# Optimization experiments

Measured on AMD Instinct MI355X. Metric: run time of the kernel, lower is better.

The kernel has to match this reference:

```python
import jax, jax.numpy as jnp
import numpy as np

NUM_HEADS = 16
GROUP_SIZE = 4
RMS_EPS = 1e-6


def _rope_cos_sin(S, head_dim):
    # matches compute_freqs_cis: freqs = 1/10000**(arange(0,hd,2)/hd), angles = outer(t, freqs)
    inv_freq = 1.0 / (10000.0 ** (jnp.arange(0, head_dim, 2, dtype=jnp.float32) / head_dim))
    t = jnp.arange(S, dtype=jnp.float32)
    angles = t[:, None] * inv_freq[None, :]          # [S, hd/2]
    return jnp.cos(angles), jnp.sin(angles)


def _apply_rope(x, cos, sin):
    # x: [B, S, h, hd]; complex multiply on (even, odd) pairs
    B, S, h, hd = x.shape
    xr = x.reshape(B, S, h, hd // 2, 2)
    x0, x1 = xr[..., 0], xr[..., 1]
    c = cos[None, :, None, :]
    s = sin[None, :, None, :]
    o0 = x0 * c - x1 * s
    o1 = x0 * s + x1 * c
    return jnp.stack([o0, o1], axis=-1).reshape(B, S, h, hd)


def setup_inputs() -> dict:
    key = jax.random.key(0)
    k1, k2, k3 = jax.random.split(key, 3)
    B, S, H = 4, 2048, 2048
    g = GROUP_SIZE
    x = jax.random.normal(k1, (B, S, H), dtype=jnp.float32)
    w_attn = jax.random.normal(k2, (H, H + 2 * H // g), dtype=jnp.float32) * 0.02
    w_proj = jax.random.normal(k3, (H, H), dtype=jnp.float32) * 0.02
    norm_w = jnp.ones((H,), dtype=jnp.float32)
    return {"x": x, "w_attn": w_attn, "w_proj": w_proj, "norm_w": norm_w}


def reference(x, w_attn, w_proj, norm_w):
    B, S, H = x.shape
    nh = NUM_HEADS
    g = GROUP_SIZE
    nkv = nh // g
    hd = H // nh
    ghd = H // g

    qkv = jnp.einsum('bsh,hf->bsf', x, w_attn)
    q = qkv[..., :H].reshape(B, S, nh, hd)
    k = qkv[..., H:H + ghd].reshape(B, S, nkv, hd)
    v = qkv[..., H + ghd:].reshape(B, S, nkv, hd)

    cos, sin = _rope_cos_sin(S, hd)
    q = _apply_rope(q, cos, sin)
    k = _apply_rope(k, cos, sin)

    q = q.transpose(0, 2, 1, 3)                      # [B, nh, S, hd]
    k = jnp.repeat(k.transpose(0, 2, 1, 3), g, axis=1)   # [B, nh, S, hd]
    v = jnp.repeat(v.transpose(0, 2, 1, 3), g, axis=1)

    scale = 1.0 / jnp.sqrt(jnp.float32(hd))
    scores = jnp.einsum('bhqd,bhkd->bhqk', q, k) * scale
    causal = jnp.tril(jnp.ones((S, S), dtype=bool))
    scores = jnp.where(causal[None, None], scores, jnp.finfo(scores.dtype).min)
    attn = jax.nn.softmax(scores, axis=-1)
    y = jnp.einsum('bhqk,bhkd->bhqd', attn, v)       # [B, nh, S, hd]
    y = y.transpose(0, 2, 1, 3).reshape(B, S, H)

    y = jnp.einsum('bsh,ho->bso', y, w_proj)
    # RMSNorm
    rms = jnp.sqrt(jnp.mean(jnp.square(y), axis=-1, keepdims=True) + RMS_EPS)
    return (y / rms) * norm_w
```

## Files before the change

kernel.cpp:

```cpp
#include <hip/hip_runtime.h>

#define DEVI __device__ __forceinline__

using u16 = unsigned short;
using u32 = unsigned int;

typedef __attribute__((ext_vector_type(8))) short short8v;
typedef __attribute__((ext_vector_type(4))) float f32x4;
typedef __attribute__((ext_vector_type(16))) float f32x16;
typedef __attribute__((ext_vector_type(2))) u32 u32x2;
typedef __attribute__((ext_vector_type(4))) u32 u32x4;

DEVI u16 f2b(float f) {
  u32 u = __builtin_bit_cast(u32, f);
  u += 0x7fffu + ((u >> 16) & 1u);
  return (u16)(u >> 16);
}
DEVI float b2f(u16 b) { return __builtin_bit_cast(float, (u32)b << 16); }

DEVI void gload16(const void* g, void* l) {
  __builtin_amdgcn_global_load_lds(
      (const __attribute__((address_space(1))) void*)g,
      (__attribute__((address_space(3))) void*)l, 16, 0, 0);
}

__global__ __launch_bounds__(256) void cvt_x_k(const float* __restrict__ in,
                                               u16* __restrict__ out) {
  size_t i = ((size_t)blockIdx.x * 256 + threadIdx.x) * 8;
  f32x4 a = *(const f32x4*)(in + i);
  f32x4 c = *(const f32x4*)(in + i + 4);
  short8v o;
  o[0] = (short)f2b(a[0]); o[1] = (short)f2b(a[1]);
  o[2] = (short)f2b(a[2]); o[3] = (short)f2b(a[3]);
  o[4] = (short)f2b(c[0]); o[5] = (short)f2b(c[1]);
  o[6] = (short)f2b(c[2]); o[7] = (short)f2b(c[3]);
  *(short8v*)(out + i) = o;
}

__global__ __launch_bounds__(256) void transpose_cvt_k(
    const float* __restrict__ in, u16* __restrict__ out, int R, int Ccols) {
  __shared__ u16 tile[64][65];
  const int r0 = blockIdx.y * 64, c0 = blockIdx.x * 64;
  const int tx = threadIdx.x & 63, ty = threadIdx.x >> 6;
#pragma unroll
  for (int jj = 0; jj < 16; ++jj) {
    int r = ty + jj * 4;
    tile[r][tx] = f2b(in[(size_t)(r0 + r) * Ccols + c0 + tx]);
  }
  __syncthreads();
#pragma unroll
  for (int jj = 0; jj < 16; ++jj) {
    int c = ty + jj * 4;
    out[(size_t)(c0 + c) * R + r0 + tx] = tile[tx][c];
  }
}

__global__ __launch_bounds__(256) void rope_table_k(float* __restrict__ cosT,
                                                    float* __restrict__ sinT) {
  int idx = blockIdx.x * 256 + threadIdx.x;
  int s = idx >> 6, i = idx & 63;
  float inv_freq = expf(-(float)i * (1.0f / 64.0f) * 9.210340371976184f);
  float ang = (float)s * inv_freq;
  cosT[idx] = cosf(ang);
  sinT[idx] = sinf(ang);
}

__global__ __launch_bounds__(256) void rope_scatter_k(
    const u16* __restrict__ qkv, const float* __restrict__ cosT,
    const float* __restrict__ sinT, u16* __restrict__ q_r,
    u16* __restrict__ k_r) {
  const float QS = 0.08838834764831845f * 1.4426950408889634f;
  const int row = blockIdx.x;
  const int b = row >> 11, s = row & 2047;
  const u16* in = qkv + (size_t)row * 3072;
  const float* cp = cosT + s * 64;
  const float* sp = sinT + s * 64;
  for (int p = threadIdx.x; p < 1280; p += 256) {
    int f0 = p * 2;
    u32 pair = *(const u32*)(in + f0);
    float x0 = b2f((u16)(pair & 0xffffu));
    float x1 = b2f((u16)(pair >> 16));
    int d, head;
    u16* dst;
    bool isq = (f0 < 2048);
    if (isq) {
      head = f0 >> 7; d = f0 & 127;
      dst = q_r + (((size_t)(b * 16 + head)) * 2048 + s) * 128 + d;
    } else {
      int idx = f0 - 2048;
      head = idx >> 7; d = idx & 127;
      dst = k_r + (((size_t)(b * 4 + head)) * 2048 + s) * 128 + d;
    }
    int i = d >> 1;
    float c = cp[i], sn = sp[i];
    float o0 = x0 * c - x1 * sn;
    float o1 = x0 * sn + x1 * c;
    if (isq) { o0 *= QS; o1 *= QS; }
    *(u32*)dst = (u32)f2b(o0) | ((u32)f2b(o1) << 16);
  }
}

__global__ __launch_bounds__(256) void v_trans_k(const u16* __restrict__ qkv,
                                                 u16* __restrict__ vT) {
  __shared__ u16 tile[64][65];
  const int s0 = blockIdx.x * 64, d0 = blockIdx.y * 64;
  const int bk = blockIdx.z;
  const int b = bk >> 2, kh = bk & 3;
  const int tx = threadIdx.x & 63, ty = threadIdx.x >> 6;
  const u16* src = qkv + ((size_t)b * 2048) * 3072 + 2560 + kh * 128;
#pragma unroll
  for (int jj = 0; jj < 16; ++jj) {
    int s = ty + jj * 4;
    tile[s][tx] = src[(size_t)(s0 + s) * 3072 + d0 + tx];
  }
  __syncthreads();
  u16* dst = vT + (((size_t)bk * 128 + d0) * 2048) + s0;
#pragma unroll
  for (int jj = 0; jj < 16; ++jj) {
    int dd = ty + jj * 4;
    dst[(size_t)dd * 2048 + tx] = tile[tx][dd];
  }
}

DEVI short8v ldf(const char* half, int r, int slot) {
  return *(const short8v*)(half + r * 64 + (((slot) ^ (r & 3)) << 4));
}

DEVI void stg(const u16* __restrict__ G, int row0, int Kd, int T, int kh,
              char* dst, int t, int w) {
#pragma unroll
  for (int i = 0; i < 2; ++i) {
    int off = i * 8192 + t * 16;
    int r = off >> 6;
    int gs = ((off >> 4) & 3) ^ (r & 3);
    gload16((const char*)G +
                (((size_t)(row0 + r) * Kd) + T * 64 + kh * 32 + gs * 8) * 2,
            dst + i * 8192 + w * 1024);
  }
}

#define VM4 asm volatile("s_waitcnt vmcnt(4)" ::: "memory")
#define PH(P2, KS, CH, STAGE_STMT, TAILWAIT)                                   \
  {                                                                            \
    if ((CH) == 0) {                                                           \
      _Pragma("unroll") for (int mt = 0; mt < 8; ++mt) af[mt] =                \
          ldf(Ab + (P2) * 32768 + (KS) * 16384, wm * 128 + mt * 16 + lo, hi);  \
    }                                                                          \
    bf0 = ldf(Bb + (P2) * 32768 + (KS) * 16384, wn * 64 + (CH) * 32 + lo, hi);\
    bf1 = ldf(Bb + (P2) * 32768 + (KS) * 16384,                                \
              wn * 64 + (CH) * 32 + 16 + lo, hi);                              \
    STAGE_STMT;                                                                \
    __builtin_amdgcn_sched_barrier(0);                                         \
    __builtin_amdgcn_s_barrier();                                              \
    asm volatile("s_waitcnt lgkmcnt(0)" ::: "memory");                         \
    __builtin_amdgcn_sched_barrier(0);                                         \
    __builtin_amdgcn_s_setprio(1);                                             \
    _Pragma("unroll") for (int mt = 0; mt < 8; ++mt) {                         \
      acc[mt][(CH) * 2] = __builtin_amdgcn_mfma_f32_16x16x32_bf16(             \
          af[mt], bf0, acc[mt][(CH) * 2], 0, 0, 0);                            \
      acc[mt][(CH) * 2 + 1] = __builtin_amdgcn_mfma_f32_16x16x32_bf16(         \
          af[mt], bf1, acc[mt][(CH) * 2 + 1], 0, 0, 0);                        \
    }                                                                          \
    __builtin_amdgcn_s_setprio(0);                                             \
    TAILWAIT;                                                                  \
    __builtin_amdgcn_sched_barrier(0);                                         \
    __builtin_amdgcn_s_barrier();                                              \
    __builtin_amdgcn_sched_barrier(0);                                         \
  }

__global__ __launch_bounds__(512, 2) void gemm256_k(const u16* __restrict__ A,
                                                    const u16* __restrict__ BT,
                                                    u16* __restrict__ C, int N,
                                                    int Kd) {
  __shared__ __align__(16) char lds[131072];
  char* Ab = lds;
  char* Bb = lds + 65536;

  const int t = threadIdx.x;
  const int lane = t & 63, lo = lane & 15, hi = lane >> 4;
  const int w = t >> 6, wm = w >> 2, wn = w & 3;

  const int ntx = gridDim.x;
  const int nwg = ntx * gridDim.y;
  const int orig = blockIdx.y * ntx + blockIdx.x;
  const int cpx = nwg >> 3;
  const int swz = (orig & 7) * cpx + (orig >> 3);
  const int m0 = (swz / ntx) * 256, n0 = (swz % ntx) * 256;

  f32x4 acc[8][4];
#pragma unroll
  for (int a = 0; a < 8; ++a)
#pragma unroll
    for (int c = 0; c < 4; ++c) acc[a][c] = (f32x4){0.f, 0.f, 0.f, 0.f};

  short8v af[8], bf0, bf1;

  const int NK = Kd >> 6;
  const int NK2 = NK >> 1;

  stg(A, m0, Kd, 0, 0, Ab + 0, t, w);
  stg(BT, n0, Kd, 0, 0, Bb + 0, t, w);
  stg(A, m0, Kd, 0, 1, Ab + 16384, t, w);
  stg(BT, n0, Kd, 0, 1, Bb + 16384, t, w);
  stg(A, m0, Kd, 1, 0, Ab + 32768, t, w);
  stg(BT, n0, Kd, 1, 0, Bb + 32768, t, w);
  VM4;
  __builtin_amdgcn_sched_barrier(0);
  __builtin_amdgcn_s_barrier();
  __builtin_amdgcn_sched_barrier(0);

  for (int kt2 = 0; kt2 < NK2; ++kt2) {
    int T1v = 2 * kt2 + 1;
    int T2v = 2 * kt2 + 2; if (T2v > NK - 1) T2v = NK - 1;
    int T3v = 2 * kt2 + 3; if (T3v > NK - 1) T3v = NK - 1;
    PH(0, 0, 0, stg(A, m0, Kd, T1v, 1, Ab + 49152, t, w), (void)0);
    PH(0, 0, 1, stg(BT, n0, Kd, T1v, 1, Bb + 49152, t, w), (void)0);
    PH(0, 1, 0, stg(A, m0, Kd, T2v, 0, Ab + 0, t, w), (void)0);
    PH(0, 1, 1, stg(BT, n0, Kd, T2v, 0, Bb + 0, t, w), VM4);
    PH(1, 0, 0, stg(A, m0, Kd, T2v, 1, Ab + 16384, t, w), (void)0);
    PH(1, 0, 1, stg(BT, n0, Kd, T2v, 1, Bb + 16384, t, w), (void)0);
    PH(1, 1, 0, stg(A, m0, Kd, T3v, 0, Ab + 32768, t, w), (void)0);
    PH(1, 1, 1, stg(BT, n0, Kd, T3v, 0, Bb + 32768, t, w), VM4);
  }
  asm volatile("s_waitcnt vmcnt(0)" ::: "memory");

#pragma unroll
  for (int mt = 0; mt < 8; ++mt)
#pragma unroll
    for (int nt = 0; nt < 4; ++nt)
#pragma unroll
      for (int r = 0; r < 4; ++r) {
        int row = m0 + wm * 128 + mt * 16 + hi * 4 + r;
        int col = n0 + wn * 64 + nt * 16 + lo;
        C[(size_t)row * N + col] = f2b(acc[mt][nt][r]);
      }
}

__global__ __launch_bounds__(256, 3) void attn_k(const u16* __restrict__ Q,
                                                 const u16* __restrict__ K,
                                                 const u16* __restrict__ VT,
                                                 u16* __restrict__ Y) {
  __shared__ __align__(16) u16 lK[2][64 * 128];
  __shared__ __align__(16) u16 lV[128 * 64];

  const int t = threadIdx.x;
  const int lane = t & 63;
  const int l31 = lane & 31, hb = lane >> 5;
  const int w = t >> 6;

  const int id = blockIdx.x;
  const int xcd = id & 7, pos = id >> 3;
  const int bh = xcd + ((pos >> 4) << 3);
  const int qt = 15 - (pos & 15);
  const int b = bh >> 4, h = bh & 15, kh = h >> 2;

  const size_t qbase = (size_t)(b * 16 + h) * 2048 * 128;
  const size_t kbase = (size_t)(b * 4 + kh) * 2048 * 128;
  const size_t vbase = (size_t)(b * 4 + kh) * 128 * 2048;

  const int q0 = qt * 128;
  const int qrow = q0 + w * 32 + l31;

  short8v qf[8];
#pragma unroll
  for (int j16 = 0; j16 < 8; ++j16)
    qf[j16] = *(const short8v*)(Q + qbase + (size_t)qrow * 128 + j16 * 16 + hb * 8);

  float m_run = -3.0e38f, l_run = 0.f;
  f32x16 oacc[4];
#pragma unroll
  for (int db = 0; db < 4; ++db)
#pragma unroll
    for (int rg = 0; rg < 16; ++rg) oacc[db][rg] = 0.f;

  const int ntile = 2 * qt + 2;

  auto stageK = [&](int buf, int j) {
    const int kv0 = j * 64;
#pragma unroll
    for (int i = 0; i < 4; ++i) {
      int off = i * 4096 + t * 16;
      int r = off >> 8;
      int sl = (off >> 4) & 15;
      int gs = sl ^ (r & 7);
      gload16((const char*)K + (kbase + (size_t)(kv0 + r) * 128 + gs * 8) * 2,
              (char*)lK[buf] + i * 4096 + w * 1024);
    }
  };
  auto stageV = [&](int j) {
    const int kv0 = j * 64;
#pragma unroll
    for (int i = 0; i < 4; ++i) {
      int off = i * 4096 + t * 16;
      int r = off >> 7;
      int sl = (off >> 4) & 7;
      int gs = sl ^ (r & 7);
      gload16((const char*)VT + (vbase + (size_t)r * 2048 + kv0 + gs * 8) * 2,
              (char*)lV + i * 4096 + w * 1024);
    }
  };

  stageK(0, 0);
  stageV(0);
  asm volatile("s_waitcnt vmcnt(0)" ::: "memory");
  __builtin_amdgcn_sched_barrier(0);
  __builtin_amdgcn_s_barrier();
  __builtin_amdgcn_sched_barrier(0);

  for (int jj = 0; jj < ntile; ++jj) {
    const int cur = jj & 1;
    const bool pre = (jj + 1 < ntile);
    if (pre) stageK(cur ^ 1, jj + 1);

    const char* lKc = (const char*)lK[cur];
    const int kv0 = jj * 64;

    f32x16 sacc[2];
#pragma unroll
    for (int kb = 0; kb < 2; ++kb)
#pragma unroll
      for (int rg = 0; rg < 16; ++rg) sacc[kb][rg] = 0.f;

    __builtin_amdgcn_s_setprio(1);
#pragma unroll
    for (int j16 = 0; j16 < 8; ++j16) {
      const int c = j16 * 2 + hb;
#pragma unroll
      for (int kb = 0; kb < 2; ++kb) {
        int kr = kb * 32 + l31;
        short8v kf = *(const short8v*)(lKc + kr * 256 + ((c ^ (kr & 7)) << 4));
        sacc[kb] = __builtin_amdgcn_mfma_f32_32x32x16_bf16(kf, qf[j16],
                                                           sacc[kb], 0, 0, 0);
      }
    }
    __builtin_amdgcn_s_setprio(0);

    if (jj >= ntile - 2) {
      const int mb = kv0 + 4 * hb - qrow;
#pragma unroll
      for (int kb = 0; kb < 2; ++kb)
#pragma unroll
        for (int rg = 0; rg < 16; ++rg)
          if (mb + kb * 32 + (rg & 3) + 8 * (rg >> 2) > 0)
            sacc[kb][rg] = -1.0e38f;
    }

    float mt0[16];
#pragma unroll
    for (int rg = 0; rg < 16; ++rg) mt0[rg] = fmaxf(sacc[0][rg], sacc[1][rg]);
#pragma unroll
    for (int rg = 0; rg < 8; ++rg) mt0[rg] = fmaxf(mt0[rg], mt0[rg + 8]);
#pragma unroll
    for (int rg = 0; rg < 4; ++rg) mt0[rg] = fmaxf(mt0[rg], mt0[rg + 4]);
    float mx = fmaxf(fmaxf(mt0[0], mt0[1]), fmaxf(mt0[2], mt0[3]));
    mx = fmaxf(mx, __shfl_xor(mx, 32, 64));

    if (__any(mx > m_run + 8.f)) {
      float mn = fmaxf(m_run, mx);
      float corr = exp2f(m_run - mn);
      m_run = mn;
      l_run *= corr;
#pragma unroll
      for (int db = 0; db < 4; ++db)
#pragma unroll
        for (int rg = 0; rg < 16; ++rg) oacc[db][rg] *= corr;
    }

    float sm0[16];
#pragma unroll
    for (int kb = 0; kb < 2; ++kb)
#pragma unroll
      for (int rg = 0; rg < 16; ++rg)
        sacc[kb][rg] = exp2f(sacc[kb][rg] - m_run);
#pragma unroll
    for (int rg = 0; rg < 16; ++rg) sm0[rg] = sacc[0][rg] + sacc[1][rg];
#pragma unroll
    for (int rg = 0; rg < 8; ++rg) sm0[rg] += sm0[rg + 8];
#pragma unroll
    for (int rg = 0; rg < 4; ++rg) sm0[rg] += sm0[rg + 4];
    float sm = (sm0[0] + sm0[1]) + (sm0[2] + sm0[3]);
    sm += __shfl_xor(sm, 32, 64);
    l_run += sm;

    short8v pa[4];
#pragma unroll
    for (int kb = 0; kb < 2; ++kb) {
      u32 pw00, pw01, pw10, pw11, pw20, pw21, pw30, pw31;
      asm("v_cvt_pk_bf16_f32 %0, %1, %2" : "=v"(pw00) : "v"(sacc[kb][0]), "v"(sacc[kb][1]));
      asm("v_cvt_pk_bf16_f32 %0, %1, %2" : "=v"(pw01) : "v"(sacc[kb][2]), "v"(sacc[kb][3]));
      asm("v_cvt_pk_bf16_f32 %0, %1, %2" : "=v"(pw10) : "v"(sacc[kb][4]), "v"(sacc[kb][5]));
      asm("v_cvt_pk_bf16_f32 %0, %1, %2" : "=v"(pw11) : "v"(sacc[kb][6]), "v"(sacc[kb][7]));
      asm("v_cvt_pk_bf16_f32 %0, %1, %2" : "=v"(pw20) : "v"(sacc[kb][8]), "v"(sacc[kb][9]));
      asm("v_cvt_pk_bf16_f32 %0, %1, %2" : "=v"(pw21) : "v"(sacc[kb][10]), "v"(sacc[kb][11]));
      asm("v_cvt_pk_bf16_f32 %0, %1, %2" : "=v"(pw30) : "v"(sacc[kb][12]), "v"(sacc[kb][13]));
      asm("v_cvt_pk_bf16_f32 %0, %1, %2" : "=v"(pw31) : "v"(sacc[kb][14]), "v"(sacc[kb][15]));
      u32x2 a0 = __builtin_amdgcn_permlane32_swap(pw00, pw10, false, false);
      u32x2 a1 = __builtin_amdgcn_permlane32_swap(pw01, pw11, false, false);
      u32x4 wv0; wv0[0] = a0[0]; wv0[1] = a1[0]; wv0[2] = a0[1]; wv0[3] = a1[1];
      pa[kb * 2 + 0] = __builtin_bit_cast(short8v, wv0);
      u32x2 b0 = __builtin_amdgcn_permlane32_swap(pw20, pw30, false, false);
      u32x2 b1 = __builtin_amdgcn_permlane32_swap(pw21, pw31, false, false);
      u32x4 wv1; wv1[0] = b0[0]; wv1[1] = b1[0]; wv1[2] = b0[1]; wv1[3] = b1[1];
      pa[kb * 2 + 1] = __builtin_bit_cast(short8v, wv1);
    }

    if (pre) { asm volatile("s_waitcnt vmcnt(4)" ::: "memory"); }
    else     { asm volatile("s_waitcnt vmcnt(0)" ::: "memory"); }
    __builtin_amdgcn_sched_barrier(0);
    __builtin_amdgcn_s_barrier();
    __builtin_amdgcn_sched_barrier(0);

    __builtin_amdgcn_s_setprio(1);
#pragma unroll
    for (int sc = 0; sc < 4; ++sc) {
      const int c = sc * 2 + hb;
#pragma unroll
      for (int db = 0; db < 4; ++db) {
        int vr = db * 32 + l31;
        short8v vf = *(const short8v*)((const char*)lV + vr * 128 +
                                       ((c ^ (vr & 7)) << 4));
        oacc[db] = __builtin_amdgcn_mfma_f32_32x32x16_bf16(vf, pa[sc],
                                                           oacc[db], 0, 0, 0);
      }
    }
    __builtin_amdgcn_s_setprio(0);

    asm volatile("s_waitcnt vmcnt(0)" ::: "memory");
    __builtin_amdgcn_sched_barrier(0);
    __builtin_amdgcn_s_barrier();
    __builtin_amdgcn_sched_barrier(0);

    if (pre) stageV(jj + 1);
  }

  const float inv = 1.0f / l_run;
  u16* yp = Y + ((size_t)b * 2048 + qrow) * 2048 + h * 128;
#pragma unroll
  for (int db = 0; db < 4; ++db)
#pragma unroll
    for (int j = 0; j < 4; ++j) {
      float a0 = oacc[db][4 * j] * inv, a1 = oacc[db][4 * j + 1] * inv;
      float a2 = oacc[db][4 * j + 2] * inv, a3 = oacc[db][4 * j + 3] * inv;
      u32 w0, w1;
      asm("v_cvt_pk_bf16_f32 %0, %1, %2" : "=v"(w0) : "v"(a0), "v"(a1));
      asm("v_cvt_pk_bf16_f32 %0, %1, %2" : "=v"(w1) : "v"(a2), "v"(a3));
      *(u32x2*)(yp + db * 32 + 8 * j + 4 * hb) = (u32x2){w0, w1};
    }
}

__global__ __launch_bounds__(256) void rmsnorm_k(const u16* __restrict__ Yb,
                                                 const float* __restrict__ nw,
                                                 float* __restrict__ out) {
  const int row = blockIdx.x;
  const int t = threadIdx.x;
  const u16* yr = Yb + (size_t)row * 2048 + t * 8;
  short8v v = *(const short8v*)yr;
  float x[8];
  float ss = 0.f;
#pragma unroll
  for (int j = 0; j < 8; ++j) {
    x[j] = b2f((u16)v[j]);
    ss += x[j] * x[j];
  }
#pragma unroll
  for (int dm = 1; dm < 64; dm <<= 1) ss += __shfl_xor(ss, dm, 64);
  __shared__ float red[4];
  if ((t & 63) == 0) red[t >> 6] = ss;
  __syncthreads();
  float tot = red[0] + red[1] + red[2] + red[3];
  float inv = rsqrtf(tot * (1.0f / 2048.0f) + 1e-6f);
  float* op = out + (size_t)row * 2048 + t * 8;
  const float* wp = nw + t * 8;
  f32x4 o0, o1;
#pragma unroll
  for (int j = 0; j < 4; ++j) o0[j] = x[j] * inv * wp[j];
#pragma unroll
  for (int j = 0; j < 4; ++j) o1[j] = x[4 + j] * inv * wp[4 + j];
  *(f32x4*)op = o0;
  *(f32x4*)(op + 4) = o1;
}

extern "C" void kernel_launch(void* const* d_in, const int* in_sizes, int n_in,
                              void* d_out, int out_size, void* d_ws,
                              size_t ws_size, hipStream_t stream) {
  (void)in_sizes; (void)n_in; (void)out_size; (void)ws_size;
  const float* x = (const float*)d_in[0];
  const float* w_attn = (const float*)d_in[1];
  const float* w_proj = (const float*)d_in[2];
  const float* norm_w = (const float*)d_in[3];
  float* out = (float*)d_out;
  char* ws = (char*)d_ws;

  size_t off = 0;
  auto alloc = [&](size_t n) {
    size_t r = off;
    off += (n + 255) & ~(size_t)255;
    return r;
  };
  u16* xb = (u16*)(ws + alloc(33554432));
  u16* wabT = (u16*)(ws + alloc(12582912));
  u16* qkv = (u16*)(ws + alloc(50331648));
  u16* q_r = (u16*)(ws + alloc(33554432));
  u16* vT = (u16*)(ws + alloc(8388608));
  u16* wpT = (u16*)(ws + alloc(8388608));
  float* cosT = (float*)(ws + alloc(524288));
  float* sinT = (float*)(ws + alloc(524288));
  u16* k_r = wabT;
  u16* y = xb;
  u16* y2 = qkv;

  cvt_x_k<<<8192, 256, 0, stream>>>(x, xb);
  transpose_cvt_k<<<dim3(48, 32), 256, 0, stream>>>(w_attn, wabT, 2048, 3072);
  transpose_cvt_k<<<dim3(32, 32), 256, 0, stream>>>(w_proj, wpT, 2048, 2048);
  rope_table_k<<<512, 256, 0, stream>>>(cosT, sinT);
  gemm256_k<<<dim3(12, 32), 512, 0, stream>>>(xb, wabT, qkv, 8192 == 0 ? 0 : 3072, 2048);
  rope_scatter_k<<<8192, 256, 0, stream>>>(qkv, cosT, sinT, q_r, k_r);
  v_trans_k<<<dim3(32, 2, 16), 256, 0, stream>>>(qkv, vT);
  attn_k<<<dim3(1024), 256, 0, stream>>>(q_r, k_r, vT, y);
  gemm256_k<<<dim3(8, 32), 512, 0, stream>>>(y, wpT, y2, 2048, 2048);
  rmsnorm_k<<<8192, 256, 0, stream>>>(y2, norm_w, out);
}
```

Baseline: 415.4 us.

## Software-pipeline PV matmul one tile behind QK in attention kernel

Double-buffers the V tile in LDS and defers each tile's P·V MFMAs to the next iteration, where they run between the QK^T score computation and the softmax. One barrier per iteration is removed, and the V load for the current tile is issued alongside the K prefetch. Because LDS use grows, launch bounds drop from 3 to 2 blocks per CU, which can lower occupancy. The dependency on the running-max correction also changes: the deferred PV for the previous tile is applied before oacc is rescaled, which keeps the result correct.

After: 408.2 us. About the same (-1.7%).

```diff
diff --git a/kernel.cpp b/kernel.cpp
--- a/kernel.cpp
+++ b/kernel.cpp
@@ -236,12 +236,12 @@
       }
 }
 
-__global__ __launch_bounds__(256, 3) void attn_k(const u16* __restrict__ Q,
+__global__ __launch_bounds__(256, 2) void attn_k(const u16* __restrict__ Q,
                                                  const u16* __restrict__ K,
                                                  const u16* __restrict__ VT,
                                                  u16* __restrict__ Y) {
   __shared__ __align__(16) u16 lK[2][64 * 128];
-  __shared__ __align__(16) u16 lV[128 * 64];
+  __shared__ __align__(16) u16 lV[2][128 * 64];
 
   const int t = threadIdx.x;
   const int lane = t & 63;
@@ -287,7 +287,7 @@
               (char*)lK[buf] + i * 4096 + w * 1024);
     }
   };
-  auto stageV = [&](int j) {
+  auto stageV = [&](int buf, int j) {
     const int kv0 = j * 64;
 #pragma unroll
     for (int i = 0; i < 4; ++i) {
@@ -296,21 +296,38 @@
       int sl = (off >> 4) & 7;
       int gs = sl ^ (r & 7);
       gload16((const char*)VT + (vbase + (size_t)r * 2048 + kv0 + gs * 8) * 2,
-              (char*)lV + i * 4096 + w * 1024);
+              (char*)lV[buf] + i * 4096 + w * 1024);
     }
   };
 
+  auto pv = [&](const char* lVc, const short8v* pa) {
+    __builtin_amdgcn_s_setprio(1);
+#pragma unroll
+    for (int sc = 0; sc < 4; ++sc) {
+      const int c = sc * 2 + hb;
+#pragma unroll
+      for (int db = 0; db < 4; ++db) {
+        int vr = db * 32 + l31;
+        short8v vf = *(const short8v*)(lVc + vr * 128 + ((c ^ (vr & 7)) << 4));
+        oacc[db] = __builtin_amdgcn_mfma_f32_32x32x16_bf16(vf, pa[sc],
+                                                           oacc[db], 0, 0, 0);
+      }
+    }
+    __builtin_amdgcn_s_setprio(0);
+  };
+
   stageK(0, 0);
-  stageV(0);
   asm volatile("s_waitcnt vmcnt(0)" ::: "memory");
   __builtin_amdgcn_sched_barrier(0);
   __builtin_amdgcn_s_barrier();
   __builtin_amdgcn_sched_barrier(0);
 
+  short8v pa_prev[4];
+
   for (int jj = 0; jj < ntile; ++jj) {
     const int cur = jj & 1;
-    const bool pre = (jj + 1 < ntile);
-    if (pre) stageK(cur ^ 1, jj + 1);
+    if (jj + 1 < ntile) stageK(cur ^ 1, jj + 1);
+    stageV(cur, jj);
 
     const char* lKc = (const char*)lK[cur];
     const int kv0 = jj * 64;
@@ -355,6 +372,8 @@
     float mx = fmaxf(fmaxf(mt0[0], mt0[1]), fmaxf(mt0[2], mt0[3]));
     mx = fmaxf(mx, __shfl_xor(mx, 32, 64));
 
+    if (jj > 0) pv((const char*)lV[cur ^ 1], pa_prev);
+
     if (__any(mx > m_run + 8.f)) {
       float mn = fmaxf(m_run, mx);
       float corr = exp2f(m_run - mn);
@@ -382,7 +401,6 @@
     sm += __shfl_xor(sm, 32, 64);
     l_run += sm;
 
-    short8v pa[4];
 #pragma unroll
     for (int kb = 0; kb < 2; ++kb) {
       u32 pw00, pw01, pw10, pw11, pw20, pw21, pw30, pw31;
@@ -397,41 +415,20 @@
       u32x2 a0 = __builtin_amdgcn_permlane32_swap(pw00, pw10, false, false);
       u32x2 a1 = __builtin_amdgcn_permlane32_swap(pw01, pw11, false, false);
       u32x4 wv0; wv0[0] = a0[0]; wv0[1] = a1[0]; wv0[2] = a0[1]; wv0[3] = a1[1];
-      pa[kb * 2 + 0] = __builtin_bit_cast(short8v, wv0);
+      pa_prev[kb * 2 + 0] = __builtin_bit_cast(short8v, wv0);
       u32x2 b0 = __builtin_amdgcn_permlane32_swap(pw20, pw30, false, false);
       u32x2 b1 = __builtin_amdgcn_permlane32_swap(pw21, pw31, false, false);
       u32x4 wv1; wv1[0] = b0[0]; wv1[1] = b1[0]; wv1[2] = b0[1]; wv1[3] = b1[1];
-      pa[kb * 2 + 1] = __builtin_bit_cast(short8v, wv1);
-    }
-
-    if (pre) { asm volatile("s_waitcnt vmcnt(4)" ::: "memory"); }
-    else     { asm volatile("s_waitcnt vmcnt(0)" ::: "memory"); }
-    __builtin_amdgcn_sched_barrier(0);
-    __builtin_amdgcn_s_barrier();
-    __builtin_amdgcn_sched_barrier(0);
-
-    __builtin_amdgcn_s_setprio(1);
-#pragma unroll
-    for (int sc = 0; sc < 4; ++sc) {
-      const int c = sc * 2 + hb;
-#pragma unroll
-      for (int db = 0; db < 4; ++db) {
-        int vr = db * 32 + l31;
-        short8v vf = *(const short8v*)((const char*)lV + vr * 128 +
-                                       ((c ^ (vr & 7)) << 4));
-        oacc[db] = __builtin_amdgcn_mfma_f32_32x32x16_bf16(vf, pa[sc],
-                                                           oacc[db], 0, 0, 0);
-      }
-    }
-    __builtin_amdgcn_s_setprio(0);
+      pa_prev[kb * 2 + 1] = __builtin_bit_cast(short8v, wv1);
+    }
 
     asm volatile("s_waitcnt vmcnt(0)" ::: "memory");
     __builtin_amdgcn_sched_barrier(0);
     __builtin_amdgcn_s_barrier();
     __builtin_amdgcn_sched_barrier(0);
-
-    if (pre) stageV(jj + 1);
-  }
+  }
+
+  pv((const char*)lV[(ntile - 1) & 1], pa_prev);
 
   const float inv = 1.0f / l_run;
   u16* yp = Y + ((size_t)b * 2048 + qrow) * 2048 + h * 128;
@@ -513,7 +510,7 @@
   transpose_cvt_k<<<dim3(48, 32), 256, 0, stream>>>(w_attn, wabT, 2048, 3072);
   transpose_cvt_k<<<dim3(32, 32), 256, 0, stream>>>(w_proj, wpT, 2048, 2048);
   rope_table_k<<<512, 256, 0, stream>>>(cosT, sinT);
-  gemm256_k<<<dim3(12, 32), 512, 0, stream>>>(xb, wabT, qkv, 8192 == 0 ? 0 : 3072, 2048);
+  gemm256_k<<<dim3(12, 32), 512, 0, stream>>>(xb, wabT, qkv, 3072, 2048);
   rope_scatter_k<<<8192, 256, 0, stream>>>(qkv, cosT, sinT, q_r, k_r);
   v_trans_k<<<dim3(32, 2, 16), 256, 0, stream>>>(qkv, vT);
   attn_k<<<dim3(1024), 256, 0, stream>>>(q_r, k_r, vT, y);
```
